# Optimization experiments

Hardware: AMD Instinct MI355X
Metric: run time of the kernel (lower is better)

## Reference

```python
import jax, jax.numpy as jnp
import numpy as np


def setup_inputs() -> dict:
    key = jax.random.key(0)
    ks = jax.random.split(key, 7)
    B, S, E = 2, 4096, 512
    return {
        "query": jax.random.normal(ks[0], (B, S, E), jnp.float32),
        "key": jax.random.normal(ks[1], (B, S, E), jnp.float32),
        "value": jax.random.normal(ks[2], (B, S, E), jnp.float32),
        "in_proj_weight": jax.random.normal(ks[3], (3 * E, E), jnp.float32) * 0.02,
        "in_proj_bias": jax.random.normal(ks[4], (3 * E,), jnp.float32) * 0.02,
        "out_proj_weight": jax.random.normal(ks[5], (E, E), jnp.float32) * 0.02,
        "out_proj_bias": jax.random.normal(ks[6], (E,), jnp.float32) * 0.02,
        "window_size": 512,
        "stride": 256,
    }


def reference(query, key, value, in_proj_weight, in_proj_bias,
              out_proj_weight, out_proj_bias, window_size, stride):
    B, S, E = query.shape
    H = 8
    hd = E // H
    scale = 1.0 / np.sqrt(hd).astype(np.float32)

    # Project full sequences once (equivalent to projecting each window slice).
    wq, wk, wv = in_proj_weight[:E], in_proj_weight[E:2 * E], in_proj_weight[2 * E:]
    bq, bk, bv = in_proj_bias[:E], in_proj_bias[E:2 * E], in_proj_bias[2 * E:]
    qp = query @ wq.T + bq   # [B,S,E]
    kp = key @ wk.T + bk
    vp = value @ wv.T + bv

    # Overlapping window gather: [nw, W] token indices.
    starts = np.arange(0, S - window_size + 1, stride)
    idx = starts[:, None] + np.arange(window_size)[None, :]  # [nw, W]
    nw, W = idx.shape

    def heads(x):  # [B,S,E] -> [B,nw,W,H,hd]
        return x[:, idx].reshape(B, nw, W, H, hd)

    qh, kh, vh = heads(qp), heads(kp), heads(vp)

    scores = jnp.einsum('bnqhd,bnkhd->bnhqk', qh, kh) * scale  # [B,nw,H,W,W]
    probs = jax.nn.softmax(scores, axis=-1)
    ctx = jnp.einsum('bnhqk,bnkhd->bnqhd', probs, vh)           # [B,nw,W,H,hd]
    ctx = ctx.reshape(B, nw * W, E)                             # concat over windows
    return ctx @ out_proj_weight.T + out_proj_bias              # [B, nw*W, E]
```

## Files before the change

### kernel.cpp

```cpp
#include <hip/hip_runtime.h>
#include <hip/hip_bf16.h>

typedef __bf16 bf16x8 __attribute__((ext_vector_type(8)));
typedef float f32x4 __attribute__((ext_vector_type(4)));
typedef float f32x16 __attribute__((ext_vector_type(16)));

__device__ __forceinline__ ushort f2bf(float f) {
  union { float f; unsigned u; } x; x.f = f;
  unsigned r = x.u + 0x7fffu + ((x.u >> 16) & 1u);
  return (ushort)(r >> 16);
}

__device__ __forceinline__ void gld_lds16(const void* g, void* l) {
  __builtin_amdgcn_global_load_lds(
      (const __attribute__((address_space(1))) void*)g,
      (__attribute__((address_space(3))) void*)l, 16, 0, 0);
}

__global__ __launch_bounds__(256) void k_cvt_all(
    const float* __restrict__ q, const float* __restrict__ k,
    const float* __restrict__ v, const float* __restrict__ wi,
    const float* __restrict__ wo, ushort* __restrict__ dst) {
  const int NQ = 1048576;
  const int NWI = 196608, NWO = 65536;
  const int total = 3 * NQ + NWI + NWO;
  int i = blockIdx.x * 256 + threadIdx.x;
  int stride = gridDim.x * 256;
  for (; i < total; i += stride) {
    const float* s; int j;
    if (i < NQ)              { s = q;  j = i; }
    else if (i < 2 * NQ)     { s = k;  j = i - NQ; }
    else if (i < 3 * NQ)     { s = v;  j = i - 2 * NQ; }
    else if (i < 3 * NQ + NWI) { s = wi; j = i - 3 * NQ; }
    else                     { s = wo; j = i - 3 * NQ - NWI; }
    float4 val = reinterpret_cast<const float4*>(s)[j];
    ushort4 o;
    o.x = f2bf(val.x); o.y = f2bf(val.y); o.z = f2bf(val.z); o.w = f2bf(val.w);
    reinterpret_cast<ushort4*>(dst)[i] = o;
  }
}

#define GK 512
#define GN 512

__global__ __launch_bounds__(256) void k_gemm(
    const ushort* __restrict__ Abase, size_t az,
    const ushort* __restrict__ Btbase, size_t bz,
    const float* __restrict__ biasbase, int biz,
    void* __restrict__ Cbase, size_t cz,
    int out_bf16, float qs)
{
  int z = blockIdx.z;
  const ushort* A  = Abase  + az * z;
  const ushort* Bt = Btbase + bz * z;
  const float* bias = biasbase + (size_t)biz * z;
  float osc = (z == 0) ? qs : 1.0f;

  __shared__ ushort As[128 * 32];
  __shared__ ushort Bs[128 * 32];

  int tid = threadIdx.x;
  int wv = tid >> 6, ln = tid & 63;
  int l15 = ln & 15, lg = ln >> 4;
  int wm = wv >> 1, wn = wv & 1;
  int m0 = blockIdx.x * 128, n0 = blockIdx.y * 128;

  f32x4 acc[4][4] = {};

  for (int kt = 0; kt < GK / 32; ++kt) {
    __syncthreads();
#pragma unroll
    for (int h2 = 0; h2 < 2; ++h2) {
      int c = h2 * 256 + wv * 64 + ln;
      int row = c >> 2, kc = (c & 3) * 8;
      gld_lds16(A  + (size_t)(m0 + row) * GK + kt * 32 + kc,
                (char*)As + (h2 * 256 + wv * 64) * 16);
      gld_lds16(Bt + (size_t)(n0 + row) * GK + kt * 32 + kc,
                (char*)Bs + (h2 * 256 + wv * 64) * 16);
    }
    __syncthreads();
    bf16x8 af[4], bf[4];
#pragma unroll
    for (int mf = 0; mf < 4; ++mf)
      af[mf] = *reinterpret_cast<const bf16x8*>(&As[(wm * 64 + mf * 16 + l15) * 32 + lg * 8]);
#pragma unroll
    for (int nf = 0; nf < 4; ++nf)
      bf[nf] = *reinterpret_cast<const bf16x8*>(&Bs[(wn * 64 + nf * 16 + l15) * 32 + lg * 8]);
#pragma unroll
    for (int mf = 0; mf < 4; ++mf)
#pragma unroll
      for (int nf = 0; nf < 4; ++nf)
        acc[mf][nf] = __builtin_amdgcn_mfma_f32_16x16x32_bf16(af[mf], bf[nf], acc[mf][nf], 0, 0, 0);
  }

#pragma unroll
  for (int mf = 0; mf < 4; ++mf)
#pragma unroll
    for (int nf = 0; nf < 4; ++nf)
#pragma unroll
      for (int r = 0; r < 4; ++r) {
        int rr = m0 + wm * 64 + mf * 16 + lg * 4 + r;
        int cc = n0 + wn * 64 + nf * 16 + l15;
        float v = (acc[mf][nf][r] + bias[cc]) * osc;
        if (out_bf16)
          ((ushort*)Cbase + cz * z)[(size_t)rr * GN + cc] = f2bf(v);
        else
          ((float*)Cbase)[(size_t)rr * GN + cc] = v;
      }
}

__global__ __launch_bounds__(256, 2) void k_attn(
    const ushort* __restrict__ qp, const ushort* __restrict__ kp,
    const ushort* __restrict__ vp, ushort* __restrict__ ctx)
{
  const int E = 512, SEQ = 4096;
  int bid0 = blockIdx.x;
  int bid = (bid0 & 7) * 60 + (bid0 >> 3);
  int qh = bid & 1;
  int h = (bid >> 1) & 7;
  int n = (bid >> 4) % 15;
  int b = bid / 240;
  int start = n * 256;

  int tid = threadIdx.x;
  int w = tid >> 6, ln = tid & 63;
  int l31 = ln & 31, hi = ln >> 5;

  size_t base = ((size_t)(b * SEQ + start)) * E + h * 64;
  const ushort* Kw = kp + base;
  const ushort* Vw = vp + base;
  const ushort* Qw = qp + base;

  __shared__ ushort Vt[32768];

  {
    int sk = (tid & 63) * 8;
    int sd = (tid >> 6) * 16;
    const ushort* src = Vw + (size_t)sk * E + sd;
    union { uint4 q[2]; ushort u[16]; } R0, R1, R2, R3, R4, R5, R6, R7;
    R0.q[0] = *(const uint4*)(src + 0 * E); R0.q[1] = *(const uint4*)(src + 0 * E + 8);
    R1.q[0] = *(const uint4*)(src + 1 * E); R1.q[1] = *(const uint4*)(src + 1 * E + 8);
    R2.q[0] = *(const uint4*)(src + 2 * E); R2.q[1] = *(const uint4*)(src + 2 * E + 8);
    R3.q[0] = *(const uint4*)(src + 3 * E); R3.q[1] = *(const uint4*)(src + 3 * E + 8);
    R4.q[0] = *(const uint4*)(src + 4 * E); R4.q[1] = *(const uint4*)(src + 4 * E + 8);
    R5.q[0] = *(const uint4*)(src + 5 * E); R5.q[1] = *(const uint4*)(src + 5 * E + 8);
    R6.q[0] = *(const uint4*)(src + 6 * E); R6.q[1] = *(const uint4*)(src + 6 * E + 8);
    R7.q[0] = *(const uint4*)(src + 7 * E); R7.q[1] = *(const uint4*)(src + 7 * E + 8);
#pragma unroll
    for (int d0 = 0; d0 < 16; ++d0) {
      int d = sd + d0;
      uint4 val;
      val.x = (uint)R0.u[d0] | ((uint)R1.u[d0] << 16);
      val.y = (uint)R2.u[d0] | ((uint)R3.u[d0] << 16);
      val.z = (uint)R4.u[d0] | ((uint)R5.u[d0] << 16);
      val.w = (uint)R6.u[d0] | ((uint)R7.u[d0] << 16);
      int off = d * 1024 + ((sk * 2) ^ ((d & 7) << 4));
      *(uint4*)((char*)Vt + off) = val;
    }
  }
  __syncthreads();

  int q0 = qh * 256 + w * 64;

  bf16x8 qa0, qa1, qa2, qa3, qb0, qb1, qb2, qb3;
  {
    const ushort* qra = Qw + (size_t)(q0 + l31) * E + hi * 8;
    const ushort* qrb = qra + (size_t)32 * E;
    qa0 = *reinterpret_cast<const bf16x8*>(qra + 0);
    qa1 = *reinterpret_cast<const bf16x8*>(qra + 16);
    qa2 = *reinterpret_cast<const bf16x8*>(qra + 32);
    qa3 = *reinterpret_cast<const bf16x8*>(qra + 48);
    qb0 = *reinterpret_cast<const bf16x8*>(qrb + 0);
    qb1 = *reinterpret_cast<const bf16x8*>(qrb + 16);
    qb2 = *reinterpret_cast<const bf16x8*>(qrb + 32);
    qb3 = *reinterpret_cast<const bf16x8*>(qrb + 48);
  }

  f32x16 ca0 = {}, ca1 = {}, cb0_ = {}, cb1_ = {};
  float psa = 0.f, psb = 0.f;
  const char* lb = (const char*)Vt;

#pragma unroll
  for (int kb = 0; kb < 16; ++kb) {
    bf16x8 kf0, kf1, kf2, kf3;
    {
      const ushort* kr = Kw + (size_t)(kb * 32 + l31) * E + hi * 8;
      kf0 = *reinterpret_cast<const bf16x8*>(kr + 0);
      kf1 = *reinterpret_cast<const bf16x8*>(kr + 16);
      kf2 = *reinterpret_cast<const bf16x8*>(kr + 32);
      kf3 = *reinterpret_cast<const bf16x8*>(kr + 48);
    }
    bf16x8 vb00, vb01, vb10, vb11;
    {
      int row = l31, rowh = 32 + l31;
      int cb0 = kb * 64 + hi * 16;
      int cb1 = cb0 + 32;
      int xr0 = (row & 7) << 4;
      vb00 = *reinterpret_cast<const bf16x8*>(lb + row * 1024 + (cb0 ^ xr0));
      vb01 = *reinterpret_cast<const bf16x8*>(lb + rowh * 1024 + (cb0 ^ xr0));
      vb10 = *reinterpret_cast<const bf16x8*>(lb + row * 1024 + (cb1 ^ xr0));
      vb11 = *reinterpret_cast<const bf16x8*>(lb + rowh * 1024 + (cb1 ^ xr0));
    }

    f32x16 s1 = {}, s2 = {};
    __builtin_amdgcn_s_setprio(1);
    s1 = __builtin_amdgcn_mfma_f32_32x32x16_bf16(kf0, qa0, s1, 0, 0, 0);
    s2 = __builtin_amdgcn_mfma_f32_32x32x16_bf16(kf0, qb0, s2, 0, 0, 0);
    s1 = __builtin_amdgcn_mfma_f32_32x32x16_bf16(kf1, qa1, s1, 0, 0, 0);
    s2 = __builtin_amdgcn_mfma_f32_32x32x16_bf16(kf1, qb1, s2, 0, 0, 0);
    s1 = __builtin_amdgcn_mfma_f32_32x32x16_bf16(kf2, qa2, s1, 0, 0, 0);
    s2 = __builtin_amdgcn_mfma_f32_32x32x16_bf16(kf2, qb2, s2, 0, 0, 0);
    s1 = __builtin_amdgcn_mfma_f32_32x32x16_bf16(kf3, qa3, s1, 0, 0, 0);
    s2 = __builtin_amdgcn_mfma_f32_32x32x16_bf16(kf3, qb3, s2, 0, 0, 0);
    __builtin_amdgcn_s_setprio(0);

#pragma unroll
    for (int r = 0; r < 16; ++r) s1[r] = __builtin_amdgcn_exp2f(s1[r]);
#pragma unroll
    for (int r = 0; r < 16; ++r) s2[r] = __builtin_amdgcn_exp2f(s2[r]);
    {
      float t0 = (s1[0] + s1[1]) + (s1[2] + s1[3]);
      float t1 = (s1[4] + s1[5]) + (s1[6] + s1[7]);
      float t2 = (s1[8] + s1[9]) + (s1[10] + s1[11]);
      float t3 = (s1[12] + s1[13]) + (s1[14] + s1[15]);
      psa += (t0 + t1) + (t2 + t3);
      float u0 = (s2[0] + s2[1]) + (s2[2] + s2[3]);
      float u1 = (s2[4] + s2[5]) + (s2[6] + s2[7]);
      float u2 = (s2[8] + s2[9]) + (s2[10] + s2[11]);
      float u3 = (s2[12] + s2[13]) + (s2[14] + s2[15]);
      psb += (u0 + u1) + (u2 + u3);
    }

    uint a0, a1, a2, a3, a4, a5, a6, a7;
    asm("v_cvt_pk_bf16_f32 %0, %1, %2" : "=v"(a0) : "v"(s1[0]),  "v"(s1[1]));
    asm("v_cvt_pk_bf16_f32 %0, %1, %2" : "=v"(a1) : "v"(s1[2]),  "v"(s1[3]));
    asm("v_cvt_pk_bf16_f32 %0, %1, %2" : "=v"(a2) : "v"(s1[4]),  "v"(s1[5]));
    asm("v_cvt_pk_bf16_f32 %0, %1, %2" : "=v"(a3) : "v"(s1[6]),  "v"(s1[7]));
    asm("v_cvt_pk_bf16_f32 %0, %1, %2" : "=v"(a4) : "v"(s1[8]),  "v"(s1[9]));
    asm("v_cvt_pk_bf16_f32 %0, %1, %2" : "=v"(a5) : "v"(s1[10]), "v"(s1[11]));
    asm("v_cvt_pk_bf16_f32 %0, %1, %2" : "=v"(a6) : "v"(s1[12]), "v"(s1[13]));
    asm("v_cvt_pk_bf16_f32 %0, %1, %2" : "=v"(a7) : "v"(s1[14]), "v"(s1[15]));
    asm("v_permlane32_swap_b32 %0, %1" : "+v"(a0), "+v"(a2));
    asm("v_permlane32_swap_b32 %0, %1" : "+v"(a1), "+v"(a3));
    asm("v_permlane32_swap_b32 %0, %1" : "+v"(a4), "+v"(a6));
    asm("v_permlane32_swap_b32 %0, %1" : "+v"(a5), "+v"(a7));
    uint b0, b1, b2, b3, b4, b5, b6, b7;
    asm("v_cvt_pk_bf16_f32 %0, %1, %2" : "=v"(b0) : "v"(s2[0]),  "v"(s2[1]));
    asm("v_cvt_pk_bf16_f32 %0, %1, %2" : "=v"(b1) : "v"(s2[2]),  "v"(s2[3]));
    asm("v_cvt_pk_bf16_f32 %0, %1, %2" : "=v"(b2) : "v"(s2[4]),  "v"(s2[5]));
    asm("v_cvt_pk_bf16_f32 %0, %1, %2" : "=v"(b3) : "v"(s2[6]),  "v"(s2[7]));
    asm("v_cvt_pk_bf16_f32 %0, %1, %2" : "=v"(b4) : "v"(s2[8]),  "v"(s2[9]));
    asm("v_cvt_pk_bf16_f32 %0, %1, %2" : "=v"(b5) : "v"(s2[10]), "v"(s2[11]));
    asm("v_cvt_pk_bf16_f32 %0, %1, %2" : "=v"(b6) : "v"(s2[12]), "v"(s2[13]));
    asm("v_cvt_pk_bf16_f32 %0, %1, %2" : "=v"(b7) : "v"(s2[14]), "v"(s2[15]));
    asm("v_permlane32_swap_b32 %0, %1" : "+v"(b0), "+v"(b2));
    asm("v_permlane32_swap_b32 %0, %1" : "+v"(b1), "+v"(b3));
    asm("v_permlane32_swap_b32 %0, %1" : "+v"(b4), "+v"(b6));
    asm("v_permlane32_swap_b32 %0, %1" : "+v"(b5), "+v"(b7));
    union { uint u[4]; bf16x8 v; } A1, A2, B1, B2;
    A1.u[0] = a0; A1.u[1] = a1; A1.u[2] = a2; A1.u[3] = a3;
    A2.u[0] = a4; A2.u[1] = a5; A2.u[2] = a6; A2.u[3] = a7;
    B1.u[0] = b0; B1.u[1] = b1; B1.u[2] = b2; B1.u[3] = b3;
    B2.u[0] = b4; B2.u[1] = b5; B2.u[2] = b6; B2.u[3] = b7;

    __builtin_amdgcn_s_setprio(1);
    ca0  = __builtin_amdgcn_mfma_f32_32x32x16_bf16(A1.v, vb00, ca0, 0, 0, 0);
    cb0_ = __builtin_amdgcn_mfma_f32_32x32x16_bf16(B1.v, vb00, cb0_, 0, 0, 0);
    ca1  = __builtin_amdgcn_mfma_f32_32x32x16_bf16(A1.v, vb01, ca1, 0, 0, 0);
    cb1_ = __builtin_amdgcn_mfma_f32_32x32x16_bf16(B1.v, vb01, cb1_, 0, 0, 0);
    ca0  = __builtin_amdgcn_mfma_f32_32x32x16_bf16(A2.v, vb10, ca0, 0, 0, 0);
    cb0_ = __builtin_amdgcn_mfma_f32_32x32x16_bf16(B2.v, vb10, cb0_, 0, 0, 0);
    ca1  = __builtin_amdgcn_mfma_f32_32x32x16_bf16(A2.v, vb11, ca1, 0, 0, 0);
    cb1_ = __builtin_amdgcn_mfma_f32_32x32x16_bf16(B2.v, vb11, cb1_, 0, 0, 0);
    __builtin_amdgcn_s_setprio(0);
  }

  psa += __shfl_xor(psa, 32);
  psb += __shfl_xor(psb, 32);
  float ria = 1.0f / psa;
  float rib = 1.0f / psb;
  size_t orow0 = (size_t)b * 7680 + (size_t)n * 512 + q0;
#pragma unroll
  for (int r = 0; r < 16; ++r) {
    int qrel = (r & 3) + 8 * (r >> 2) + 4 * hi;
    float r1 = __shfl(ria, qrel);
    float r2 = __shfl(rib, qrel);
    ushort* dA = ctx + (orow0 + qrel) * E + h * 64 + l31;
    ushort* dB = ctx + (orow0 + 32 + qrel) * E + h * 64 + l31;
    dA[0]  = f2bf(ca0[r] * r1);
    dA[32] = f2bf(ca1[r] * r1);
    dB[0]  = f2bf(cb0_[r] * r2);
    dB[32] = f2bf(cb1_[r] * r2);
  }
}

extern "C" void kernel_launch(void* const* d_in, const int* in_sizes, int n_in,
                              void* d_out, int out_size, void* d_ws, size_t ws_size,
                              hipStream_t stream) {
  const float* query = (const float*)d_in[0];
  const float* key   = (const float*)d_in[1];
  const float* value = (const float*)d_in[2];
  const float* ipw   = (const float*)d_in[3];
  const float* ipb   = (const float*)d_in[4];
  const float* opw   = (const float*)d_in[5];
  const float* opb   = (const float*)d_in[6];

  ushort* qb  = (ushort*)d_ws;
  ushort* kb  = qb  + 4194304;
  ushort* vb  = kb  + 4194304;
  ushort* wib = vb  + 4194304;
  ushort* wob = wib + 786432;
  ushort* qp  = wob + 262144;
  ushort* kp  = qp  + 4194304;
  ushort* vp  = kp  + 4194304;
  ushort* ctx = vp  + 4194304;

  const float SC = 0.125f * 1.44269504088896340736f;

  k_cvt_all<<<2048, 256, 0, stream>>>(query, key, value, ipw, opw, qb);

  k_gemm<<<dim3(64, 4, 3), 256, 0, stream>>>(
      qb, (size_t)4194304, wib, (size_t)262144, ipb, 512,
      (void*)qp, (size_t)4194304, 1, SC);

  k_attn<<<480, 256, 0, stream>>>(qp, kp, vp, ctx);

  k_gemm<<<dim3(120, 4, 1), 256, 0, stream>>>(
      ctx, (size_t)0, wob, (size_t)0, opb, 0,
      d_out, (size_t)0, 0, 1.0f);
}
```

Baseline: 87.75 us.

## Fuse fp32-to-bf16 activation conversion into the input projection GEMM load

The separate pre-pass that converted query/key/value to bf16 is removed. The input projection GEMM now reads fp32 activations directly, converts them with packed bf16 conversion instructions, and stores them into shared memory. Only the weights are still converted in a small kernel. This drops a full write and re-read of three bf16 activation copies. In exchange the A loads become synchronous register loads instead of async global-to-LDS copies, which may expose more latency in the GEMM main loop.

```diff
diff --git a/kernel.cpp b/kernel.cpp
--- a/kernel.cpp
+++ b/kernel.cpp
@@ -17,22 +17,17 @@
       (__attribute__((address_space(3))) void*)l, 16, 0, 0);
 }
 
-__global__ __launch_bounds__(256) void k_cvt_all(
-    const float* __restrict__ q, const float* __restrict__ k,
-    const float* __restrict__ v, const float* __restrict__ wi,
-    const float* __restrict__ wo, ushort* __restrict__ dst) {
-  const int NQ = 1048576;
+__global__ __launch_bounds__(256) void k_cvt_w(
+    const float* __restrict__ wi, const float* __restrict__ wo,
+    ushort* __restrict__ dst) {
   const int NWI = 196608, NWO = 65536;
-  const int total = 3 * NQ + NWI + NWO;
+  const int total = NWI + NWO;
   int i = blockIdx.x * 256 + threadIdx.x;
   int stride = gridDim.x * 256;
   for (; i < total; i += stride) {
     const float* s; int j;
-    if (i < NQ)              { s = q;  j = i; }
-    else if (i < 2 * NQ)     { s = k;  j = i - NQ; }
-    else if (i < 3 * NQ)     { s = v;  j = i - 2 * NQ; }
-    else if (i < 3 * NQ + NWI) { s = wi; j = i - 3 * NQ; }
-    else                     { s = wo; j = i - 3 * NQ - NWI; }
+    if (i < NWI) { s = wi; j = i; }
+    else         { s = wo; j = i - NWI; }
     float4 val = reinterpret_cast<const float4*>(s)[j];
     ushort4 o;
     o.x = f2bf(val.x); o.y = f2bf(val.y); o.z = f2bf(val.z); o.w = f2bf(val.w);
@@ -44,14 +39,17 @@
 #define GN 512
 
 __global__ __launch_bounds__(256) void k_gemm(
-    const ushort* __restrict__ Abase, size_t az,
+    const ushort* __restrict__ Ab,
+    const float* __restrict__ za0,
+    const float* __restrict__ za1,
+    const float* __restrict__ za2,
     const ushort* __restrict__ Btbase, size_t bz,
     const float* __restrict__ biasbase, int biz,
     void* __restrict__ Cbase, size_t cz,
-    int out_bf16, float qs)
+    int out_bf16, float qs, int a_f32)
 {
   int z = blockIdx.z;
-  const ushort* A  = Abase  + az * z;
+  const float* A32 = (z == 0) ? za0 : (z == 1) ? za1 : za2;
   const ushort* Bt = Btbase + bz * z;
   const float* bias = biasbase + (size_t)biz * z;
   float osc = (z == 0) ? qs : 1.0f;
@@ -73,10 +71,38 @@
     for (int h2 = 0; h2 < 2; ++h2) {
       int c = h2 * 256 + wv * 64 + ln;
       int row = c >> 2, kc = (c & 3) * 8;
-      gld_lds16(A  + (size_t)(m0 + row) * GK + kt * 32 + kc,
-                (char*)As + (h2 * 256 + wv * 64) * 16);
       gld_lds16(Bt + (size_t)(n0 + row) * GK + kt * 32 + kc,
                 (char*)Bs + (h2 * 256 + wv * 64) * 16);
+    }
+    if (a_f32) {
+      int row = tid >> 1, kh = (tid & 1) * 16;
+      const float* af = A32 + (size_t)(m0 + row) * GK + kt * 32 + kh;
+      float4 f0 = reinterpret_cast<const float4*>(af)[0];
+      float4 f1 = reinterpret_cast<const float4*>(af)[1];
+      float4 f2 = reinterpret_cast<const float4*>(af)[2];
+      float4 f3 = reinterpret_cast<const float4*>(af)[3];
+      uint w0, w1, w2, w3, w4, w5, w6, w7;
+      asm("v_cvt_pk_bf16_f32 %0, %1, %2" : "=v"(w0) : "v"(f0.x), "v"(f0.y));
+      asm("v_cvt_pk_bf16_f32 %0, %1, %2" : "=v"(w1) : "v"(f0.z), "v"(f0.w));
+      asm("v_cvt_pk_bf16_f32 %0, %1, %2" : "=v"(w2) : "v"(f1.x), "v"(f1.y));
+      asm("v_cvt_pk_bf16_f32 %0, %1, %2" : "=v"(w3) : "v"(f1.z), "v"(f1.w));
+      asm("v_cvt_pk_bf16_f32 %0, %1, %2" : "=v"(w4) : "v"(f2.x), "v"(f2.y));
+      asm("v_cvt_pk_bf16_f32 %0, %1, %2" : "=v"(w5) : "v"(f2.z), "v"(f2.w));
+      asm("v_cvt_pk_bf16_f32 %0, %1, %2" : "=v"(w6) : "v"(f3.x), "v"(f3.y));
+      asm("v_cvt_pk_bf16_f32 %0, %1, %2" : "=v"(w7) : "v"(f3.z), "v"(f3.w));
+      char* dst = (char*)As + ((size_t)row * 32 + kh) * 2;
+      uint4 p0; p0.x = w0; p0.y = w1; p0.z = w2; p0.w = w3;
+      uint4 p1; p1.x = w4; p1.y = w5; p1.z = w6; p1.w = w7;
+      reinterpret_cast<uint4*>(dst)[0] = p0;
+      reinterpret_cast<uint4*>(dst)[1] = p1;
+    } else {
+#pragma unroll
+      for (int h2 = 0; h2 < 2; ++h2) {
+        int c = h2 * 256 + wv * 64 + ln;
+        int row = c >> 2, kc = (c & 3) * 8;
+        gld_lds16(Ab + (size_t)(m0 + row) * GK + kt * 32 + kc,
+                  (char*)As + (h2 * 256 + wv * 64) * 16);
+      }
     }
     __syncthreads();
     bf16x8 af[4], bf[4];
@@ -305,10 +331,7 @@
   const float* opw   = (const float*)d_in[5];
   const float* opb   = (const float*)d_in[6];
 
-  ushort* qb  = (ushort*)d_ws;
-  ushort* kb  = qb  + 4194304;
-  ushort* vb  = kb  + 4194304;
-  ushort* wib = vb  + 4194304;
+  ushort* wib = (ushort*)d_ws;
   ushort* wob = wib + 786432;
   ushort* qp  = wob + 262144;
   ushort* kp  = qp  + 4194304;
@@ -317,15 +340,17 @@
 
   const float SC = 0.125f * 1.44269504088896340736f;
 
-  k_cvt_all<<<2048, 256, 0, stream>>>(query, key, value, ipw, opw, qb);
+  k_cvt_w<<<512, 256, 0, stream>>>(ipw, opw, wib);
 
   k_gemm<<<dim3(64, 4, 3), 256, 0, stream>>>(
-      qb, (size_t)4194304, wib, (size_t)262144, ipb, 512,
-      (void*)qp, (size_t)4194304, 1, SC);
+      nullptr, query, key, value,
+      wib, (size_t)262144, ipb, 512,
+      (void*)qp, (size_t)4194304, 1, SC, 1);
 
   k_attn<<<480, 256, 0, stream>>>(qp, kp, vp, ctx);
 
   k_gemm<<<dim3(120, 4, 1), 256, 0, stream>>>(
-      ctx, (size_t)0, wob, (size_t)0, opb, 0,
-      d_out, (size_t)0, 0, 1.0f);
-}
+      ctx, nullptr, nullptr, nullptr,
+      wob, (size_t)0, opb, 0,
+      d_out, (size_t)0, 0, 1.0f, 0);
+}
```

Result: no change. 86.88 us (-1.0%).

## Fuse fp32-to-bf16 activation conversion into weight-stationary projection GEMMs

Applied to the files above, without the earlier changes.

Drops the separate conversion pass over query/key/value. The in-projection GEMM now reads fp32 activations straight from global memory and converts them in registers with v_cvt_pk_bf16_f32. Both GEMMs are restructured to be weight-stationary: each block keeps a full 64x512 swizzled weight slab in LDS and streams A fragments directly from global without LDS staging. Blocks are remapped to spread work across XCDs. The aim is to remove an extra read/write round trip of 12M elements and the per-k-tile barriers, at the cost of 64KB LDS per block and uncoalesced direct A loads.

```diff
diff --git a/kernel.cpp b/kernel.cpp
--- a/kernel.cpp
+++ b/kernel.cpp
@@ -17,22 +17,17 @@
       (__attribute__((address_space(3))) void*)l, 16, 0, 0);
 }
 
-__global__ __launch_bounds__(256) void k_cvt_all(
-    const float* __restrict__ q, const float* __restrict__ k,
-    const float* __restrict__ v, const float* __restrict__ wi,
-    const float* __restrict__ wo, ushort* __restrict__ dst) {
-  const int NQ = 1048576;
+__global__ __launch_bounds__(256) void k_cvt_w(
+    const float* __restrict__ wi, const float* __restrict__ wo,
+    ushort* __restrict__ dst) {
   const int NWI = 196608, NWO = 65536;
-  const int total = 3 * NQ + NWI + NWO;
+  const int total = NWI + NWO;
   int i = blockIdx.x * 256 + threadIdx.x;
   int stride = gridDim.x * 256;
   for (; i < total; i += stride) {
     const float* s; int j;
-    if (i < NQ)              { s = q;  j = i; }
-    else if (i < 2 * NQ)     { s = k;  j = i - NQ; }
-    else if (i < 3 * NQ)     { s = v;  j = i - 2 * NQ; }
-    else if (i < 3 * NQ + NWI) { s = wi; j = i - 3 * NQ; }
-    else                     { s = wo; j = i - 3 * NQ - NWI; }
+    if (i < NWI) { s = wi; j = i; }
+    else         { s = wo; j = i - NWI; }
     float4 val = reinterpret_cast<const float4*>(s)[j];
     ushort4 o;
     o.x = f2bf(val.x); o.y = f2bf(val.y); o.z = f2bf(val.z); o.w = f2bf(val.w);
@@ -40,72 +35,95 @@
   }
 }
 
-#define GK 512
-#define GN 512
-
-__global__ __launch_bounds__(256) void k_gemm(
-    const ushort* __restrict__ Abase, size_t az,
-    const ushort* __restrict__ Btbase, size_t bz,
-    const float* __restrict__ biasbase, int biz,
-    void* __restrict__ Cbase, size_t cz,
-    int out_bf16, float qs)
+template <int AF32>
+__global__ __launch_bounds__(256, 2) void k_gemm_ws(
+    const float* __restrict__ a32_0, const float* __restrict__ a32_1,
+    const float* __restrict__ a32_2, const ushort* __restrict__ ab16,
+    const ushort* __restrict__ Wbase, const float* __restrict__ biasbase,
+    void* __restrict__ Cbase, float qs, int nx, int q8)
 {
-  int z = blockIdx.z;
-  const ushort* A  = Abase  + az * z;
-  const ushort* Bt = Btbase + bz * z;
-  const float* bias = biasbase + (size_t)biz * z;
-  float osc = (z == 0) ? qs : 1.0f;
-
-  __shared__ ushort As[128 * 32];
-  __shared__ ushort Bs[128 * 32];
+  int bid0 = blockIdx.x;
+  int bid = (bid0 & 7) * q8 + (bid0 >> 3);
+  int yy = bid & 7;
+  int rest = bid >> 3;
+  int xx = rest % nx;
+  int z = rest / nx;
 
   int tid = threadIdx.x;
   int wv = tid >> 6, ln = tid & 63;
   int l15 = ln & 15, lg = ln >> 4;
-  int wm = wv >> 1, wn = wv & 1;
-  int m0 = blockIdx.x * 128, n0 = blockIdx.y * 128;
+
+  int n0 = yy * 64;
+  int m0 = xx * 256 + wv * 64;
+
+  const float* A32 = (z == 0) ? a32_0 : (z == 1) ? a32_1 : a32_2;
+  const ushort* Wt = Wbase + (size_t)262144 * z + (size_t)n0 * 512;
+  const float* bias = biasbase + 512 * z;
+  float osc = (AF32 && z == 0) ? qs : 1.0f;
+
+  __shared__ ushort Bs[64 * 512];
+
+#pragma unroll
+  for (int c = 0; c < 16; ++c) {
+    int s = c * 256 + tid;
+    int row = s >> 6;
+    int cs = (s & 63) * 16;
+    int kb = (cs ^ ((row & 7) << 4)) >> 1;
+    gld_lds16(Wt + (size_t)row * 512 + kb,
+              (char*)Bs + (c * 256 + wv * 64) * 16);
+  }
+  __syncthreads();
 
   f32x4 acc[4][4] = {};
 
-  for (int kt = 0; kt < GK / 32; ++kt) {
-    __syncthreads();
-#pragma unroll
-    for (int h2 = 0; h2 < 2; ++h2) {
-      int c = h2 * 256 + wv * 64 + ln;
-      int row = c >> 2, kc = (c & 3) * 8;
-      gld_lds16(A  + (size_t)(m0 + row) * GK + kt * 32 + kc,
-                (char*)As + (h2 * 256 + wv * 64) * 16);
-      gld_lds16(Bt + (size_t)(n0 + row) * GK + kt * 32 + kc,
-                (char*)Bs + (h2 * 256 + wv * 64) * 16);
-    }
-    __syncthreads();
-    bf16x8 af[4], bf[4];
+#pragma unroll
+  for (int kt = 0; kt < 16; ++kt) {
+    bf16x8 af[4], wf[4];
+#pragma unroll
+    for (int mf = 0; mf < 4; ++mf) {
+      if (AF32) {
+        const float* ap = A32 + (size_t)(m0 + mf * 16 + l15) * 512 + kt * 32 + lg * 8;
+        float4 x0 = reinterpret_cast<const float4*>(ap)[0];
+        float4 x1 = reinterpret_cast<const float4*>(ap)[1];
+        uint w0, w1, w2, w3;
+        asm("v_cvt_pk_bf16_f32 %0, %1, %2" : "=v"(w0) : "v"(x0.x), "v"(x0.y));
+        asm("v_cvt_pk_bf16_f32 %0, %1, %2" : "=v"(w1) : "v"(x0.z), "v"(x0.w));
+        asm("v_cvt_pk_bf16_f32 %0, %1, %2" : "=v"(w2) : "v"(x1.x), "v"(x1.y));
+        asm("v_cvt_pk_bf16_f32 %0, %1, %2" : "=v"(w3) : "v"(x1.z), "v"(x1.w));
+        union { uint u[4]; bf16x8 v; } t;
+        t.u[0] = w0; t.u[1] = w1; t.u[2] = w2; t.u[3] = w3;
+        af[mf] = t.v;
+      } else {
+        af[mf] = *reinterpret_cast<const bf16x8*>(
+            ab16 + (size_t)(m0 + mf * 16 + l15) * 512 + kt * 32 + lg * 8);
+      }
+    }
+#pragma unroll
+    for (int nf = 0; nf < 4; ++nf) {
+      int row = nf * 16 + l15;
+      int off = (kt * 64 + lg * 16) ^ ((row & 7) << 4);
+      wf[nf] = *reinterpret_cast<const bf16x8*>((const char*)Bs + row * 1024 + off);
+    }
 #pragma unroll
     for (int mf = 0; mf < 4; ++mf)
-      af[mf] = *reinterpret_cast<const bf16x8*>(&As[(wm * 64 + mf * 16 + l15) * 32 + lg * 8]);
+#pragma unroll
+      for (int nf = 0; nf < 4; ++nf)
+        acc[mf][nf] = __builtin_amdgcn_mfma_f32_16x16x32_bf16(af[mf], wf[nf], acc[mf][nf], 0, 0, 0);
+  }
+
+#pragma unroll
+  for (int mf = 0; mf < 4; ++mf)
 #pragma unroll
     for (int nf = 0; nf < 4; ++nf)
-      bf[nf] = *reinterpret_cast<const bf16x8*>(&Bs[(wn * 64 + nf * 16 + l15) * 32 + lg * 8]);
-#pragma unroll
-    for (int mf = 0; mf < 4; ++mf)
-#pragma unroll
-      for (int nf = 0; nf < 4; ++nf)
-        acc[mf][nf] = __builtin_amdgcn_mfma_f32_16x16x32_bf16(af[mf], bf[nf], acc[mf][nf], 0, 0, 0);
-  }
-
-#pragma unroll
-  for (int mf = 0; mf < 4; ++mf)
-#pragma unroll
-    for (int nf = 0; nf < 4; ++nf)
 #pragma unroll
       for (int r = 0; r < 4; ++r) {
-        int rr = m0 + wm * 64 + mf * 16 + lg * 4 + r;
-        int cc = n0 + wn * 64 + nf * 16 + l15;
+        int rr = m0 + mf * 16 + lg * 4 + r;
+        int cc = n0 + nf * 16 + l15;
         float v = (acc[mf][nf][r] + bias[cc]) * osc;
-        if (out_bf16)
-          ((ushort*)Cbase + cz * z)[(size_t)rr * GN + cc] = f2bf(v);
+        if (AF32)
+          ((ushort*)Cbase + (size_t)4194304 * z)[(size_t)rr * 512 + cc] = f2bf(v);
         else
-          ((float*)Cbase)[(size_t)rr * GN + cc] = v;
+          ((float*)Cbase)[(size_t)rr * 512 + cc] = v;
       }
 }
 
@@ -305,10 +323,7 @@
   const float* opw   = (const float*)d_in[5];
   const float* opb   = (const float*)d_in[6];
 
-  ushort* qb  = (ushort*)d_ws;
-  ushort* kb  = qb  + 4194304;
-  ushort* vb  = kb  + 4194304;
-  ushort* wib = vb  + 4194304;
+  ushort* wib = (ushort*)d_ws;
   ushort* wob = wib + 786432;
   ushort* qp  = wob + 262144;
   ushort* kp  = qp  + 4194304;
@@ -317,15 +332,13 @@
 
   const float SC = 0.125f * 1.44269504088896340736f;
 
-  k_cvt_all<<<2048, 256, 0, stream>>>(query, key, value, ipw, opw, qb);
-
-  k_gemm<<<dim3(64, 4, 3), 256, 0, stream>>>(
-      qb, (size_t)4194304, wib, (size_t)262144, ipb, 512,
-      (void*)qp, (size_t)4194304, 1, SC);
+  k_cvt_w<<<512, 256, 0, stream>>>(ipw, opw, wib);
+
+  k_gemm_ws<1><<<768, 256, 0, stream>>>(
+      query, key, value, nullptr, wib, ipb, (void*)qp, SC, 32, 96);
 
   k_attn<<<480, 256, 0, stream>>>(qp, kp, vp, ctx);
 
-  k_gemm<<<dim3(120, 4, 1), 256, 0, stream>>>(
-      ctx, (size_t)0, wob, (size_t)0, opb, 0,
-      d_out, (size_t)0, 0, 1.0f);
-}
+  k_gemm_ws<0><<<480, 256, 0, stream>>>(
+      nullptr, nullptr, nullptr, ctx, wob, opb, d_out, 1.0f, 60, 60);
+}
```

Measured after the change: 125.4 us. 42.9% more time.
